# Kernel optimization log

Measured on AMD Instinct MI355X. Metric: run time of the kernel, lower is better.

The kernel has to match this reference:

```python
import jax, jax.numpy as jnp
import numpy as np
import math

B, N, IN_DIM, HID, OUT = 16, 1024, 3, 32, 4
RATIO = 0.2
K1 = math.ceil(RATIO * N)    # 205 nodes kept after pool 1
K2 = math.ceil(RATIO * K1)   # 41 nodes kept after pool 2
AVG_DEG = 16.0
BN_EPS = 1e-5


def setup_inputs() -> dict:
    key = jax.random.key(0)
    ks = jax.random.split(key, 16)
    x = jax.random.normal(ks[0], (B, N, IN_DIM), jnp.float32)
    # sparse random undirected adjacency (binary edge weights = 1), no self loops
    u = jax.random.uniform(ks[1], (B, N, N))
    A = (u < (AVG_DEG / N)).astype(jnp.float32)
    A = jnp.maximum(A, jnp.swapaxes(A, -1, -2))
    A = A * (1.0 - jnp.eye(N, dtype=jnp.float32))
    g = lambda i, shp: (jax.random.normal(ks[i], shp, jnp.float32) * 0.1)
    params = dict(
        Wd0=g(2, (IN_DIM, HID)), bd0=jnp.zeros((HID,), jnp.float32),
        Wd1=g(3, (HID, HID)),    bd1=jnp.zeros((HID,), jnp.float32),
        Wd2=g(4, (HID, HID)),    bd2=jnp.zeros((HID,), jnp.float32),
        Wu0=g(5, (HID, HID)),    bu0=jnp.zeros((HID,), jnp.float32),
        Wu1=g(6, (HID, HID)),    bu1=jnp.zeros((HID,), jnp.float32),
        p1=g(7, (HID,)), p2=g(8, (HID,)),
        gamma=jnp.ones((HID,), jnp.float32), beta=jnp.zeros((HID,), jnp.float32),
        W1=g(9, (HID, HID)),  b1=jnp.zeros((HID,), jnp.float32),
        W2=g(10, (HID, HID)), b2=jnp.zeros((HID,), jnp.float32),
        W3=g(11, (HID, OUT)), b3=jnp.zeros((OUT,), jnp.float32),
    )
    return {"x": x, "adj": A, **params}


def _gcn(A, x, W, b):
    # GCNConv(improved=True): A_hat = A + 2I, symmetric normalization
    n = A.shape[-1]
    A_hat = A + 2.0 * jnp.eye(n, dtype=A.dtype)
    deg = A_hat.sum(-1)                              # [B, n]
    dis = jnp.where(deg > 0, jax.lax.rsqrt(deg), 0.0)
    A_norm = dis[..., :, None] * A_hat * dis[..., None, :]
    return jnp.einsum('bij,bjf->bif', A_norm, x @ W) + b


def _augment(A):
    # GraphUNet.augment_adj: add self loops (w=1), square adjacency, drop diag
    n = A.shape[-1]
    eye = jnp.eye(n, dtype=A.dtype)
    Bm = A + eye
    A2 = jnp.einsum('bij,bjk->bik', Bm, Bm)
    return A2 * (1.0 - eye)


def _topk_pool(A, x, p, k):
    # TopKPooling: score = tanh(x.p / ||p||), keep top-k nodes per graph
    score = jnp.tanh((x @ p) / jnp.linalg.norm(p))   # [B, n]
    vals, perm = jax.lax.top_k(score, k)             # descending, matches PyG
    bidx = jnp.arange(x.shape[0])[:, None]
    x_p = x[bidx, perm] * vals[..., None]
    A_p = A[bidx[..., None], perm[:, :, None], perm[:, None, :]]
    return A_p, x_p, perm


def reference(x, adj, Wd0, bd0, Wd1, bd1, Wd2, bd2, Wu0, bu0, Wu1, bu1,
              p1, p2, gamma, beta, W1, b1, W2, b2, W3, b3):
    bidx = jnp.arange(x.shape[0])[:, None]
    # ---- GraphUNet down path ----
    h0 = jax.nn.relu(_gcn(adj, x, Wd0, bd0))
    A1, h, perm1 = _topk_pool(_augment(adj), h0, p1, K1)
    h1 = jax.nn.relu(_gcn(A1, h, Wd1, bd1))
    A2, h, perm2 = _topk_pool(_augment(A1), h1, p2, K2)
    h = jax.nn.relu(_gcn(A2, h, Wd2, bd2))
    # ---- up path (sum_res=True) ----
    up = jnp.zeros_like(h1).at[bidx, perm2].set(h)
    h = jax.nn.relu(_gcn(A1, h1 + up, Wu0, bu0))
    up = jnp.zeros_like(h0).at[bidx, perm1].set(h)
    h = _gcn(adj, h0 + up, Wu1, bu1)   # last up conv: no activation
    # ---- BatchNorm1d over all nodes (training-mode batch stats, biased var) ----
    mean = h.mean((0, 1))
    var = h.var((0, 1))
    hn = (h - mean) * jax.lax.rsqrt(var + BN_EPS) * gamma + beta
    # ---- outnetwork MLP (dropout = identity in eval), LeakyReLU slope 0.01 ----
    r = jax.nn.leaky_relu(hn @ W1 + b1)
    r = jax.nn.leaky_relu(r @ W2 + b2)
    r = r @ W3 + b3
    return r.at[..., 0].set(jax.nn.sigmoid(r[..., 0]))
```

## Files before the change

kernel.cpp:

```cpp
#include <hip/hip_runtime.h>
#include <cmath>

#define BB 16
#define NN 1024
#define KK1 205
#define KK2 42
#define CAP 96
#define CHUNKS1 52

__global__ void k_deg_csr(const float* __restrict__ adj, const float* __restrict__ x,
                          const float* __restrict__ W,
                          float* __restrict__ dis0, int* __restrict__ ncnt,
                          int* __restrict__ nbr, unsigned long long* __restrict__ mask,
                          float* __restrict__ dxw) {
  int row = blockIdx.x * 4 + (threadIdx.x >> 6);
  int lane = threadIdx.x & 63;
  const float* ar = adj + (size_t)row * NN;
  float v[16];
#pragma unroll
  for (int c = 0; c < 16; ++c) v[c] = ar[c * 64 + lane];
  int base = 0;
  int* nr = nbr + (size_t)row * CAP;
#pragma unroll
  for (int c = 0; c < 16; ++c) {
    unsigned long long m = __ballot(v[c] != 0.0f);
    if (lane == c) mask[(size_t)row * 16 + c] = m;
    if (v[c] != 0.0f) {
      int pos = base + __popcll(m & ((1ull << lane) - 1ull));
      if (pos < CAP) nr[pos] = c * 64 + lane;
    }
    base += __popcll(m);
  }
  float dis = rsqrtf((float)base + 2.0f);
  if (lane == 0) {
    ncnt[row] = base < CAP ? base : CAP;
    dis0[row] = dis;
  }
  if (lane < 32) {
    float x0 = x[row * 3], x1 = x[row * 3 + 1], x2 = x[row * 3 + 2];
    float s = x0 * W[lane] + x1 * W[32 + lane] + x2 * W[64 + lane];
    dxw[(size_t)row * 32 + lane] = s * dis;
  }
}

template<bool RELU, bool SCORE, bool BNSTATS>
__global__ void k_spmm(const float* __restrict__ dxw, const float* __restrict__ dis,
                       const int* __restrict__ ncnt, const int* __restrict__ nbr,
                       const float* __restrict__ bias, float* __restrict__ out,
                       float* __restrict__ score, const float* __restrict__ p,
                       float* __restrict__ pacc) {
  int tid = threadIdx.x;
  int g = tid >> 5, f = tid & 31;
  int node = blockIdx.x * 8 + g;
  int b = node >> 10;
  int cnt = ncnt[node];
  const int* lst = nbr + (size_t)node * CAP;
  const float* dbase = dxw + ((size_t)(b << 10) << 5);
  float a0 = 0.f, a1 = 0.f, a2 = 0.f, a3 = 0.f;
  int k = 0;
  for (; k + 4 <= cnt; k += 4) {
    int4 j4 = *(const int4*)(lst + k);
    a0 += dbase[(size_t)j4.x * 32 + f];
    a1 += dbase[(size_t)j4.y * 32 + f];
    a2 += dbase[(size_t)j4.z * 32 + f];
    a3 += dbase[(size_t)j4.w * 32 + f];
  }
  for (; k < cnt; ++k) a0 += dbase[(size_t)lst[k] * 32 + f];
  float acc = (a0 + a1) + (a2 + a3);
  acc += 2.0f * dxw[(size_t)node * 32 + f];
  float r = dis[node] * acc + bias[f];
  if (RELU) r = fmaxf(r, 0.f);
  out[(size_t)node * 32 + f] = r;
  if (SCORE) {
    float pv = p[f];
    float d = r * pv, pp = pv * pv;
#pragma unroll
    for (int o = 16; o; o >>= 1) { d += __shfl_xor(d, o, 32); pp += __shfl_xor(pp, o, 32); }
    if (f == 0) score[node] = tanhf(d / sqrtf(pp));
  }
  if (BNSTATS) {
    __shared__ float bs[8][32], bq[8][32];
    bs[g][f] = r; bq[g][f] = r * r;
    __syncthreads();
    if (tid < 32) {
      float S = 0.f, Q = 0.f;
#pragma unroll
      for (int q = 0; q < 8; ++q) { S += bs[q][tid]; Q += bq[q][tid]; }
      atomicAdd(&pacc[tid], S);
      atomicAdd(&pacc[32 + tid], Q);
    }
  }
}

__global__ __launch_bounds__(256) void k_sortA1(
    const unsigned long long* __restrict__ mask, const float* __restrict__ score1,
    const float* __restrict__ h0, const float* __restrict__ Wd1,
    float* __restrict__ A1, float* __restrict__ dis1, float* __restrict__ t1,
    int* __restrict__ inv1) {
  __shared__ union {
    unsigned long long skey[1024];
    unsigned long long smT[16 * KK1];
  } sm;
  __shared__ int sp[KK1];
  __shared__ float sval[KK1];
  int blk = blockIdx.x;
  int b = blk / CHUNKS1, chunk = blk - b * CHUNKS1;
  int t = threadIdx.x;
  for (int idx = t; idx < 1024; idx += 256) {
    float v = score1[b * NN + idx];
    unsigned int u = __float_as_uint(v);
    if (u == 0x80000000u) u = 0u;
    unsigned int ordv = (u & 0x80000000u) ? ~u : (u | 0x80000000u);
    if (chunk == 0) inv1[b * NN + idx] = -1;
    sm.skey[idx] = ((unsigned long long)(~ordv) << 32) | (unsigned)idx;
  }
  __syncthreads();
  for (int k = 2; k <= 1024; k <<= 1)
    for (int j = k >> 1; j > 0; j >>= 1) {
      for (int idx = t; idx < 1024; idx += 256) {
        int ixj = idx ^ j;
        if (ixj > idx) {
          unsigned long long a = sm.skey[idx], c = sm.skey[ixj];
          bool up = ((idx & k) == 0);
          if (up == (a > c)) { sm.skey[idx] = c; sm.skey[ixj] = a; }
        }
      }
      __syncthreads();
    }
  if (t < KK1) {
    unsigned long long kk = sm.skey[t];
    unsigned int ord = ~(unsigned int)(kk >> 32);
    unsigned int u = (ord & 0x80000000u) ? (ord & 0x7FFFFFFFu) : ~ord;
    int src = (int)(kk & 0xFFFFFFFFull);
    sp[t] = src;
    sval[t] = __uint_as_float(u);
    if (chunk == 0) inv1[b * NN + src] = t;
  }
  __syncthreads();
  for (int q = t; q < KK1 * 16; q += 256) {
    int i = q >> 4, w = q & 15;
    sm.smT[w * KK1 + i] = mask[((size_t)(b * NN + sp[i])) * 16 + w];
  }
  __syncthreads();
  int wave = t >> 6, lane = t & 63;
  int i = chunk * 4 + wave;
  if (i < KK1) {
    unsigned long long r[16];
#pragma unroll
    for (int w = 0; w < 16; ++w) r[w] = sm.smT[w * KK1 + i];
    float rowsum = 0.f;
    for (int j = lane; j < KK1; j += 64) {
      int cnt = 0;
#pragma unroll
      for (int w = 0; w < 16; ++w) cnt += __popcll(r[w] & sm.smT[w * KK1 + j]);
      int pj = sp[j];
      float edge = (float)((r[pj >> 6] >> (pj & 63)) & 1ull);
      float v = (j == i) ? 0.f : ((float)cnt + 2.f * edge);
      A1[((size_t)(b * KK1) + i) * KK1 + j] = v;
      rowsum += v;
    }
#pragma unroll
    for (int o = 32; o; o >>= 1) rowsum += __shfl_xor(rowsum, o);
    float dis = rsqrtf(rowsum + 2.0f);
    if (lane == 0) dis1[b * KK1 + i] = dis;
    if (lane < 32) {
      const float* hr = h0 + (size_t)(b * NN + sp[i]) * 32;
      float s = 0.f;
#pragma unroll
      for (int k = 0; k < 32; ++k) s += hr[k] * Wd1[k * 32 + lane];
      t1[((size_t)(b * KK1) + i) * 32 + lane] = s * dis * sval[i];
    }
  }
}

template<bool RELU, bool SCORE>
__global__ __launch_bounds__(256) void k_dense_apply(
    const float* __restrict__ A, const float* __restrict__ tbuf,
    const float* __restrict__ dis, const float* __restrict__ bias,
    int M, float* __restrict__ out, float* __restrict__ score,
    const float* __restrict__ p) {
  int row = blockIdx.x;
  int b = row / M, i = row - b * M;
  int tid = threadIdx.x;
  int g = tid >> 5, f = tid & 31;
  const float* Ar = A + (size_t)row * M;
  const float* tb = tbuf + (size_t)b * M * 32;
  float acc = 0.f;
  for (int j = g; j < M; j += 8)
    acc += Ar[j] * tb[j * 32 + f];
  __shared__ float ls[8][32];
  ls[g][f] = acc;
  __syncthreads();
  if (tid < 32) {
    float s = 0.f;
#pragma unroll
    for (int q = 0; q < 8; ++q) s += ls[q][tid];
    s += 2.0f * tb[i * 32 + tid];
    float r = dis[row] * s + bias[tid];
    if (RELU) r = fmaxf(r, 0.f);
    out[(size_t)row * 32 + tid] = r;
    if (SCORE) {
      float pv = p[tid];
      float d = r * pv, pp = pv * pv;
#pragma unroll
      for (int o = 16; o; o >>= 1) { d += __shfl_xor(d, o, 32); pp += __shfl_xor(pp, o, 32); }
      if (tid == 0) score[row] = tanhf(d / sqrtf(pp));
    }
  }
}

__global__ __launch_bounds__(256) void k_buildA2s(
    const float* __restrict__ score2, const float* __restrict__ A1,
    const float* __restrict__ h1, const float* __restrict__ Wd2,
    float* __restrict__ A2, float* __restrict__ dis2, float* __restrict__ t2,
    int* __restrict__ inv2) {
  __shared__ unsigned long long skey[256];
  __shared__ int sp2[KK2];
  __shared__ float sv2[KK2];
  __shared__ float gsum[8];
  __shared__ float ds2s;
  int row = blockIdx.x;
  int b = row / KK2, i = row - b * KK2;
  int t = threadIdx.x;
  {
    unsigned int ordv;
    if (t < KK1) {
      float v = score2[b * KK1 + t];
      unsigned int u = __float_as_uint(v);
      if (u == 0x80000000u) u = 0u;
      ordv = (u & 0x80000000u) ? ~u : (u | 0x80000000u);
      if (i == 0) inv2[b * KK1 + t] = -1;
    } else ordv = 0u;
    skey[t] = ((unsigned long long)(~ordv) << 32) | (unsigned)t;
  }
  __syncthreads();
  for (int k = 2; k <= 256; k <<= 1)
    for (int j = k >> 1; j > 0; j >>= 1) {
      int ixj = t ^ j;
      if (ixj > t) {
        unsigned long long a = skey[t], c = skey[ixj];
        bool up = ((t & k) == 0);
        if (up == (a > c)) { skey[t] = c; skey[ixj] = a; }
      }
      __syncthreads();
    }
  if (t < KK2) {
    unsigned long long kk = skey[t];
    unsigned int ord = ~(unsigned int)(kk >> 32);
    unsigned int u = (ord & 0x80000000u) ? (ord & 0x7FFFFFFFu) : ~ord;
    int src = (int)(kk & 0xFFFFFFFFull);
    sp2[t] = src;
    sv2[t] = __uint_as_float(u);
    if (i == 0) inv2[b * KK1 + src] = t;
  }
  __syncthreads();
  int g = t >> 5, lane = t & 31;
  int pi = sp2[i];
  const float* Ri = A1 + ((size_t)(b * KK1 + pi)) * KK1;
  float part = 0.f;
  for (int j = g; j < KK2; j += 8) {
    const float* Rj = A1 + ((size_t)(b * KK1 + sp2[j])) * KK1;
    float s = 0.f;
    for (int k = lane; k < KK1; k += 32) s += Ri[k] * Rj[k];
#pragma unroll
    for (int o = 16; o; o >>= 1) s += __shfl_xor(s, o, 32);
    float v = (i == j) ? 0.f : (s + 2.0f * Ri[sp2[j]]);
    if (lane == 0) {
      A2[(size_t)row * KK2 + j] = v;
      part += v;
    }
  }
  if (lane == 0) gsum[g] = part;
  __syncthreads();
  if (t == 0) {
    float s = 0.f;
#pragma unroll
    for (int q = 0; q < 8; ++q) s += gsum[q];
    float d2 = rsqrtf(s + 2.0f);
    dis2[row] = d2;
    ds2s = d2;
  }
  __syncthreads();
  if (t < 32) {
    const float* hr = h1 + (size_t)(b * KK1 + pi) * 32;
    float s = 0.f;
#pragma unroll
    for (int k = 0; k < 32; ++k) s += hr[k] * Wd2[k * 32 + t];
    t2[(size_t)row * 32 + t] = s * ds2s * sv2[i];
  }
}

__global__ void k_xw32u(const float* __restrict__ h, const float* __restrict__ up,
                        const int* __restrict__ inv, const float* __restrict__ W,
                        const float* __restrict__ dis, int M, int K,
                        float* __restrict__ out, float* __restrict__ pacc) {
  if (pacc && blockIdx.x == 0 && threadIdx.x < 64) pacc[threadIdx.x] = 0.f;
  int idx = blockIdx.x * 256 + threadIdx.x;
  int f = idx & 31; int node = idx >> 5;
  int b = node / M;
  int iv = inv[node];
  const float* xr = h + (size_t)node * 32;
  float s = 0.f;
  if (iv >= 0) {
    const float* ur = up + (size_t)(b * K + iv) * 32;
#pragma unroll
    for (int k = 0; k < 32; ++k) s += (xr[k] + ur[k]) * W[k * 32 + f];
  } else {
#pragma unroll
    for (int k = 0; k < 32; ++k) s += xr[k] * W[k * 32 + f];
  }
  out[idx] = s * dis[node];
}

__global__ __launch_bounds__(64) void k_mlp(
    const float* __restrict__ h, const float* __restrict__ pacc,
    const float* __restrict__ gamma, const float* __restrict__ beta,
    const float* __restrict__ W1, const float* __restrict__ b1,
    const float* __restrict__ W2, const float* __restrict__ b2,
    const float* __restrict__ W3, const float* __restrict__ b3,
    float* __restrict__ out) {
  __shared__ float sW1[1024], sW2[1024], sW3[128];
  __shared__ float sb1[32], sb2[32], sb3[4], sscale[32], sshift[32];
  int t = threadIdx.x;
  {
    const float4* W1v = (const float4*)W1; float4* d1 = (float4*)sW1;
#pragma unroll
    for (int i = 0; i < 4; ++i) d1[t + i * 64] = W1v[t + i * 64];
    const float4* W2v = (const float4*)W2; float4* d2 = (float4*)sW2;
#pragma unroll
    for (int i = 0; i < 4; ++i) d2[t + i * 64] = W2v[t + i * 64];
    if (t < 32) ((float4*)sW3)[t] = ((const float4*)W3)[t];
    if (t < 32) { sb1[t] = b1[t]; sb2[t] = b2[t]; }
    if (t < 4) sb3[t] = b3[t];
    if (t < 32) {
      const float inv = 1.0f / (float)(BB * NN);
      float m = pacc[t] * inv;
      float v = pacc[32 + t] * inv - m * m;
      float sc = gamma[t] * rsqrtf(v + 1e-5f);
      sscale[t] = sc;
      sshift[t] = beta[t] - m * sc;
    }
  }
  __syncthreads();
  int node = blockIdx.x * 64 + t;
  const float4* hr = (const float4*)(h + (size_t)node * 32);
  float hn[32];
#pragma unroll
  for (int i = 0; i < 8; ++i) {
    float4 x = hr[i];
    hn[i * 4 + 0] = x.x * sscale[i * 4 + 0] + sshift[i * 4 + 0];
    hn[i * 4 + 1] = x.y * sscale[i * 4 + 1] + sshift[i * 4 + 1];
    hn[i * 4 + 2] = x.z * sscale[i * 4 + 2] + sshift[i * 4 + 2];
    hn[i * 4 + 3] = x.w * sscale[i * 4 + 3] + sshift[i * 4 + 3];
  }
  float r1[32];
#pragma unroll
  for (int f = 0; f < 32; ++f) r1[f] = sb1[f];
#pragma unroll
  for (int k = 0; k < 32; ++k) {
    float a = hn[k];
#pragma unroll
    for (int f = 0; f < 32; ++f) r1[f] += a * sW1[k * 32 + f];
  }
#pragma unroll
  for (int f = 0; f < 32; ++f) r1[f] = r1[f] > 0.f ? r1[f] : 0.01f * r1[f];
  float r2[32];
#pragma unroll
  for (int f = 0; f < 32; ++f) r2[f] = sb2[f];
#pragma unroll
  for (int k = 0; k < 32; ++k) {
    float a = r1[k];
#pragma unroll
    for (int f = 0; f < 32; ++f) r2[f] += a * sW2[k * 32 + f];
  }
#pragma unroll
  for (int f = 0; f < 32; ++f) r2[f] = r2[f] > 0.f ? r2[f] : 0.01f * r2[f];
  float r3[4];
#pragma unroll
  for (int c = 0; c < 4; ++c) r3[c] = sb3[c];
#pragma unroll
  for (int k = 0; k < 32; ++k) {
    float a = r2[k];
#pragma unroll
    for (int c = 0; c < 4; ++c) r3[c] += a * sW3[k * 4 + c];
  }
  float4 o;
  o.x = 1.0f / (1.0f + expf(-r3[0]));
  o.y = r3[1]; o.z = r3[2]; o.w = r3[3];
  ((float4*)out)[node] = o;
}

extern "C" void kernel_launch(void* const* d_in, const int* in_sizes, int n_in,
                              void* d_out, int out_size, void* d_ws, size_t ws_size,
                              hipStream_t stream) {
  const float* x    = (const float*)d_in[0];
  const float* adj  = (const float*)d_in[1];
  const float* Wd0  = (const float*)d_in[2];
  const float* bd0  = (const float*)d_in[3];
  const float* Wd1  = (const float*)d_in[4];
  const float* bd1  = (const float*)d_in[5];
  const float* Wd2  = (const float*)d_in[6];
  const float* bd2  = (const float*)d_in[7];
  const float* Wu0  = (const float*)d_in[8];
  const float* bu0  = (const float*)d_in[9];
  const float* Wu1  = (const float*)d_in[10];
  const float* bu1  = (const float*)d_in[11];
  const float* p1   = (const float*)d_in[12];
  const float* p2   = (const float*)d_in[13];
  const float* gamma= (const float*)d_in[14];
  const float* beta = (const float*)d_in[15];
  const float* W1   = (const float*)d_in[16];
  const float* b1   = (const float*)d_in[17];
  const float* W2   = (const float*)d_in[18];
  const float* b2   = (const float*)d_in[19];
  const float* W3   = (const float*)d_in[20];
  const float* b3   = (const float*)d_in[21];
  float* out = (float*)d_out;

  char* w = (char*)d_ws;
  auto alloc = [&](size_t bytes) -> void* {
    void* p = (void*)w;
    w += (bytes + 255) & ~(size_t)255;
    return p;
  };
  float* dis0 = (float*)alloc(BB * NN * 4);
  int*   ncnt = (int*)alloc(BB * NN * 4);
  int*   nbr  = (int*)alloc((size_t)BB * NN * CAP * 4);
  unsigned long long* mask = (unsigned long long*)alloc((size_t)BB * NN * 16 * 8);
  float* dxw  = (float*)alloc((size_t)BB * NN * 32 * 4);
  float* h0   = (float*)alloc((size_t)BB * NN * 32 * 4);
  float* score1 = (float*)alloc(BB * NN * 4);
  int*   inv1 = (int*)alloc(BB * NN * 4);
  float* A1   = (float*)alloc((size_t)BB * KK1 * KK1 * 4);
  float* dis1 = (float*)alloc(BB * KK1 * 4);
  float* t1   = (float*)alloc((size_t)BB * KK1 * 32 * 4);
  float* h1   = (float*)alloc((size_t)BB * KK1 * 32 * 4);
  float* score2 = (float*)alloc(BB * KK1 * 4);
  int*   inv2 = (int*)alloc(BB * KK1 * 4);
  float* A2   = (float*)alloc((size_t)BB * KK2 * KK2 * 4);
  float* dis2 = (float*)alloc(BB * KK2 * 4);
  float* t2   = (float*)alloc((size_t)BB * KK2 * 32 * 4);
  float* h2   = (float*)alloc((size_t)BB * KK2 * 32 * 4);
  float* hu0  = (float*)alloc((size_t)BB * KK1 * 32 * 4);
  float* hfin = (float*)alloc((size_t)BB * NN * 32 * 4);
  float* pacc = (float*)alloc(64 * 4);

  const int TOT_N32  = BB * NN * 32;
  const int TOT_K132 = BB * KK1 * 32;

  k_deg_csr<<<BB * NN / 4, 256, 0, stream>>>(adj, x, Wd0, dis0, ncnt, nbr, mask, dxw);
  k_spmm<true, true, false><<<BB * NN / 8, 256, 0, stream>>>(
      dxw, dis0, ncnt, nbr, bd0, h0, score1, p1, nullptr);
  k_sortA1<<<BB * CHUNKS1, 256, 0, stream>>>(mask, score1, h0, Wd1, A1, dis1, t1, inv1);
  k_dense_apply<true, true><<<BB * KK1, 256, 0, stream>>>(
      A1, t1, dis1, bd1, KK1, h1, score2, p2);
  k_buildA2s<<<BB * KK2, 256, 0, stream>>>(score2, A1, h1, Wd2, A2, dis2, t2, inv2);
  k_dense_apply<true, false><<<BB * KK2, 256, 0, stream>>>(
      A2, t2, dis2, bd2, KK2, h2, nullptr, nullptr);
  k_xw32u<<<TOT_K132 / 256, 256, 0, stream>>>(h1, h2, inv2, Wu0, dis1, KK1, KK2, t1, nullptr);
  k_dense_apply<true, false><<<BB * KK1, 256, 0, stream>>>(
      A1, t1, dis1, bu0, KK1, hu0, nullptr, nullptr);
  k_xw32u<<<TOT_N32 / 256, 256, 0, stream>>>(h0, hu0, inv1, Wu1, dis0, NN, KK1, dxw, pacc);
  k_spmm<false, false, true><<<BB * NN / 8, 256, 0, stream>>>(
      dxw, dis0, ncnt, nbr, bu1, hfin, nullptr, nullptr, pacc);
  k_mlp<<<BB * NN / 64, 64, 0, stream>>>(hfin, pacc, gamma, beta,
                                         W1, b1, W2, b2, W3, b3, out);
}
```

Baseline: 351.5 us.

## Stage per-graph features in LDS for SpMM and replicate BN stat accumulators

The SpMM kernel now copies a whole graph's 1024x32 feature matrix (128 KB) into shared memory, and each block handles 64 nodes, so neighbor gathers come from LDS instead of global memory. BatchNorm statistics are accumulated per thread over 8 nodes and then atomically added into 64 replicated partial buffers to cut atomic contention. The MLP kernel sums those replicas, and zeroing moves into the first kernel. The cost is that the grid shrinks from 2048 to 256 blocks, and the 128 KB of LDS per block allows only one block per CU. Each block also pays a full 128 KB copy before it can start.

```diff
diff --git a/kernel.cpp b/kernel.cpp
--- a/kernel.cpp
+++ b/kernel.cpp
@@ -7,12 +7,16 @@
 #define KK2 42
 #define CAP 96
 #define CHUNKS1 52
+#define NREP 64
 
 __global__ void k_deg_csr(const float* __restrict__ adj, const float* __restrict__ x,
                           const float* __restrict__ W,
                           float* __restrict__ dis0, int* __restrict__ ncnt,
                           int* __restrict__ nbr, unsigned long long* __restrict__ mask,
-                          float* __restrict__ dxw) {
+                          float* __restrict__ dxw, float* __restrict__ pacc) {
+  if (blockIdx.x == 0) {
+    for (int q = threadIdx.x; q < NREP * 64; q += 256) pacc[q] = 0.f;
+  }
   int row = blockIdx.x * 4 + (threadIdx.x >> 6);
   int lane = threadIdx.x & 63;
   const float* ar = adj + (size_t)row * NN;
@@ -44,50 +48,64 @@
 }
 
 template<bool RELU, bool SCORE, bool BNSTATS>
-__global__ void k_spmm(const float* __restrict__ dxw, const float* __restrict__ dis,
-                       const int* __restrict__ ncnt, const int* __restrict__ nbr,
-                       const float* __restrict__ bias, float* __restrict__ out,
-                       float* __restrict__ score, const float* __restrict__ p,
-                       float* __restrict__ pacc) {
+__global__ __launch_bounds__(256) void k_spmm_lds(
+    const float* __restrict__ dxw, const float* __restrict__ dis,
+    const int* __restrict__ ncnt, const int* __restrict__ nbr,
+    const float* __restrict__ bias, float* __restrict__ out,
+    float* __restrict__ score, const float* __restrict__ p,
+    float* __restrict__ pacc) {
+  __shared__ float sdxw[NN * 32];
+  __shared__ float bs[8][32], bq[8][32];
   int tid = threadIdx.x;
+  int b = blockIdx.x >> 4, chunk = blockIdx.x & 15;
+  {
+    const float4* src = (const float4*)(dxw + ((size_t)b * NN) * 32);
+    float4* dst = (float4*)sdxw;
+    for (int q = tid; q < NN * 8; q += 256) dst[q] = src[q];
+  }
+  __syncthreads();
   int g = tid >> 5, f = tid & 31;
-  int node = blockIdx.x * 8 + g;
-  int b = node >> 10;
-  int cnt = ncnt[node];
-  const int* lst = nbr + (size_t)node * CAP;
-  const float* dbase = dxw + ((size_t)(b << 10) << 5);
-  float a0 = 0.f, a1 = 0.f, a2 = 0.f, a3 = 0.f;
-  int k = 0;
-  for (; k + 4 <= cnt; k += 4) {
-    int4 j4 = *(const int4*)(lst + k);
-    a0 += dbase[(size_t)j4.x * 32 + f];
-    a1 += dbase[(size_t)j4.y * 32 + f];
-    a2 += dbase[(size_t)j4.z * 32 + f];
-    a3 += dbase[(size_t)j4.w * 32 + f];
-  }
-  for (; k < cnt; ++k) a0 += dbase[(size_t)lst[k] * 32 + f];
-  float acc = (a0 + a1) + (a2 + a3);
-  acc += 2.0f * dxw[(size_t)node * 32 + f];
-  float r = dis[node] * acc + bias[f];
-  if (RELU) r = fmaxf(r, 0.f);
-  out[(size_t)node * 32 + f] = r;
-  if (SCORE) {
-    float pv = p[f];
-    float d = r * pv, pp = pv * pv;
-#pragma unroll
-    for (int o = 16; o; o >>= 1) { d += __shfl_xor(d, o, 32); pp += __shfl_xor(pp, o, 32); }
-    if (f == 0) score[node] = tanhf(d / sqrtf(pp));
+  float bia = bias[f];
+  float pv = SCORE ? p[f] : 0.f;
+  float S = 0.f, Q = 0.f;
+#pragma unroll
+  for (int it = 0; it < 8; ++it) {
+    int li = chunk * 64 + g * 8 + it;
+    int node = b * NN + li;
+    int cnt = ncnt[node];
+    const int* lst = nbr + (size_t)node * CAP;
+    float a0 = 0.f, a1 = 0.f, a2 = 0.f, a3 = 0.f;
+    int k = 0;
+    for (; k + 4 <= cnt; k += 4) {
+      int4 j4 = *(const int4*)(lst + k);
+      a0 += sdxw[j4.x * 32 + f];
+      a1 += sdxw[j4.y * 32 + f];
+      a2 += sdxw[j4.z * 32 + f];
+      a3 += sdxw[j4.w * 32 + f];
+    }
+    for (; k < cnt; ++k) a0 += sdxw[lst[k] * 32 + f];
+    float acc = (a0 + a1) + (a2 + a3) + 2.0f * sdxw[li * 32 + f];
+    float r = dis[node] * acc + bia;
+    if (RELU) r = fmaxf(r, 0.f);
+    out[(size_t)node * 32 + f] = r;
+    if (SCORE) {
+      float d = r * pv, pp = pv * pv;
+#pragma unroll
+      for (int o = 16; o; o >>= 1) { d += __shfl_xor(d, o, 32); pp += __shfl_xor(pp, o, 32); }
+      if (f == 0) score[node] = tanhf(d / sqrtf(pp));
+    }
+    if (BNSTATS) { S += r; Q += r * r; }
   }
   if (BNSTATS) {
-    __shared__ float bs[8][32], bq[8][32];
-    bs[g][f] = r; bq[g][f] = r * r;
+    bs[g][f] = S; bq[g][f] = Q;
     __syncthreads();
     if (tid < 32) {
-      float S = 0.f, Q = 0.f;
-#pragma unroll
-      for (int q = 0; q < 8; ++q) { S += bs[q][tid]; Q += bq[q][tid]; }
-      atomicAdd(&pacc[tid], S);
-      atomicAdd(&pacc[32 + tid], Q);
+      float SS = 0.f, QQ = 0.f;
+#pragma unroll
+      for (int q = 0; q < 8; ++q) { SS += bs[q][tid]; QQ += bq[q][tid]; }
+      int rep = blockIdx.x & (NREP - 1);
+      atomicAdd(&pacc[rep * 64 + tid], SS);
+      atomicAdd(&pacc[rep * 64 + 32 + tid], QQ);
     }
   }
 }
@@ -293,8 +311,7 @@
 __global__ void k_xw32u(const float* __restrict__ h, const float* __restrict__ up,
                         const int* __restrict__ inv, const float* __restrict__ W,
                         const float* __restrict__ dis, int M, int K,
-                        float* __restrict__ out, float* __restrict__ pacc) {
-  if (pacc && blockIdx.x == 0 && threadIdx.x < 64) pacc[threadIdx.x] = 0.f;
+                        float* __restrict__ out) {
   int idx = blockIdx.x * 256 + threadIdx.x;
   int f = idx & 31; int node = idx >> 5;
   int b = node / M;
@@ -321,6 +338,7 @@
     float* __restrict__ out) {
   __shared__ float sW1[1024], sW2[1024], sW3[128];
   __shared__ float sb1[32], sb2[32], sb3[4], sscale[32], sshift[32];
+  __shared__ float red[64];
   int t = threadIdx.x;
   {
     const float4* W1v = (const float4*)W1; float4* d1 = (float4*)sW1;
@@ -332,14 +350,22 @@
     if (t < 32) ((float4*)sW3)[t] = ((const float4*)W3)[t];
     if (t < 32) { sb1[t] = b1[t]; sb2[t] = b2[t]; }
     if (t < 4) sb3[t] = b3[t];
-    if (t < 32) {
-      const float inv = 1.0f / (float)(BB * NN);
-      float m = pacc[t] * inv;
-      float v = pacc[32 + t] * inv - m * m;
-      float sc = gamma[t] * rsqrtf(v + 1e-5f);
-      sscale[t] = sc;
-      sshift[t] = beta[t] - m * sc;
-    }
+    float a0 = 0.f, a1 = 0.f, a2 = 0.f, a3 = 0.f;
+#pragma unroll
+    for (int rep = 0; rep < NREP; rep += 4) {
+      a0 += pacc[(rep + 0) * 64 + t]; a1 += pacc[(rep + 1) * 64 + t];
+      a2 += pacc[(rep + 2) * 64 + t]; a3 += pacc[(rep + 3) * 64 + t];
+    }
+    red[t] = (a0 + a1) + (a2 + a3);
+  }
+  __syncthreads();
+  if (t < 32) {
+    const float inv = 1.0f / (float)(BB * NN);
+    float m = red[t] * inv;
+    float v = red[32 + t] * inv - m * m;
+    float sc = gamma[t] * rsqrtf(v + 1e-5f);
+    sscale[t] = sc;
+    sshift[t] = beta[t] - m * sc;
   }
   __syncthreads();
   int node = blockIdx.x * 64 + t;
@@ -443,13 +469,13 @@
   float* h2   = (float*)alloc((size_t)BB * KK2 * 32 * 4);
   float* hu0  = (float*)alloc((size_t)BB * KK1 * 32 * 4);
   float* hfin = (float*)alloc((size_t)BB * NN * 32 * 4);
-  float* pacc = (float*)alloc(64 * 4);
+  float* pacc = (float*)alloc((size_t)NREP * 64 * 4);
 
   const int TOT_N32  = BB * NN * 32;
   const int TOT_K132 = BB * KK1 * 32;
 
-  k_deg_csr<<<BB * NN / 4, 256, 0, stream>>>(adj, x, Wd0, dis0, ncnt, nbr, mask, dxw);
-  k_spmm<true, true, false><<<BB * NN / 8, 256, 0, stream>>>(
+  k_deg_csr<<<BB * NN / 4, 256, 0, stream>>>(adj, x, Wd0, dis0, ncnt, nbr, mask, dxw, pacc);
+  k_spmm_lds<true, true, false><<<BB * 16, 256, 0, stream>>>(
       dxw, dis0, ncnt, nbr, bd0, h0, score1, p1, nullptr);
   k_sortA1<<<BB * CHUNKS1, 256, 0, stream>>>(mask, score1, h0, Wd1, A1, dis1, t1, inv1);
   k_dense_apply<true, true><<<BB * KK1, 256, 0, stream>>>(
@@ -457,11 +483,11 @@
   k_buildA2s<<<BB * KK2, 256, 0, stream>>>(score2, A1, h1, Wd2, A2, dis2, t2, inv2);
   k_dense_apply<true, false><<<BB * KK2, 256, 0, stream>>>(
       A2, t2, dis2, bd2, KK2, h2, nullptr, nullptr);
-  k_xw32u<<<TOT_K132 / 256, 256, 0, stream>>>(h1, h2, inv2, Wu0, dis1, KK1, KK2, t1, nullptr);
+  k_xw32u<<<TOT_K132 / 256, 256, 0, stream>>>(h1, h2, inv2, Wu0, dis1, KK1, KK2, t1);
   k_dense_apply<true, false><<<BB * KK1, 256, 0, stream>>>(
       A1, t1, dis1, bu0, KK1, hu0, nullptr, nullptr);
-  k_xw32u<<<TOT_N32 / 256, 256, 0, stream>>>(h0, hu0, inv1, Wu1, dis0, NN, KK1, dxw, pacc);
-  k_spmm<false, false, true><<<BB * NN / 8, 256, 0, stream>>>(
+  k_xw32u<<<TOT_N32 / 256, 256, 0, stream>>>(h0, hu0, inv1, Wu1, dis0, NN, KK1, dxw);
+  k_spmm_lds<false, false, true><<<BB * 16, 256, 0, stream>>>(
       dxw, dis0, ncnt, nbr, bu1, hfin, nullptr, nullptr, pacc);
   k_mlp<<<BB * NN / 64, 64, 0, stream>>>(hfin, pacc, gamma, beta,
                                          W1, b1, W2, b2, W3, b3, out);
```

Result: faster. 343.1 us (-2.4%).
